# Kernel optimization log

Hardware: AMD Instinct MI355X
Metric: run time of the kernel (lower is better)

## Reference

```python
import jax, jax.numpy as jnp
import numpy as np

T, N, D_OBS = 32, 32, 64
HID, HEADS, MEM, N_ACT = 512, 4, 128, 16
SECTIONS = [HEADS * HID, HEADS, HID, 1, HID, HID, HEADS, 1, 1, 3 * HEADS]
XI = sum(SECTIONS)


def setup_inputs() -> dict:
    key = jax.random.key(0)
    ks = jax.random.split(key, 8)
    s = 0.02
    return {
        "inputs": jax.random.normal(ks[0], (T, N, D_OBS), jnp.float32),
        "w_ih": jax.random.normal(ks[1], (3 * HID, D_OBS), jnp.float32) * s,
        "w_hh": jax.random.normal(ks[2], (3 * HID, HID), jnp.float32) * s,
        "b_ih": jnp.zeros((3 * HID,), jnp.float32),
        "b_hh": jnp.zeros((3 * HID,), jnp.float32),
        "Wf": jax.random.normal(ks[3], (XI, HID), jnp.float32) * s,
        "bf": jnp.zeros((XI,), jnp.float32),
        "Wa": jax.random.normal(ks[4], (N_ACT, HID), jnp.float32) * s,
        "ba": jnp.zeros((N_ACT,), jnp.float32),
        "Wc": jax.random.normal(ks[5], (1, HID), jnp.float32) * s,
        "bc": jnp.zeros((1,), jnp.float32),
    }


def reference(inputs, w_ih, w_hh, b_ih, b_hh, Wf, bf, Wa, ba, Wc, bc):
    idx = np.cumsum(SECTIONS)[:-1]
    eps = 1e-8

    def step(carry, x_t):
        h, wr, u, ww, M, p, L = carry
        # --- GRU cell (torch convention) ---
        gi = x_t @ w_ih.T + b_ih
        gh = h @ w_hh.T + b_hh
        ir, iz, inn = jnp.split(gi, 3, axis=-1)
        hr, hz, hn = jnp.split(gh, 3, axis=-1)
        rg = jax.nn.sigmoid(ir + hr)
        zg = jax.nn.sigmoid(iz + hz)
        ng = jnp.tanh(inn + rg * hn)
        h = (1 - zg) * ng + zg * h
        # --- interface vector xi ---
        xi = jax.nn.relu(h) @ Wf.T + bf
        Kr, Br, kw, bw, e, v, F_hat, ga, gw, Pi = jnp.split(xi, idx, axis=-1)
        Kr = Kr.reshape(N, HEADS, HID)
        Br = jax.nn.softplus(Br)                      # [N,H]
        bw = jax.nn.softplus(bw)                      # [N,1]
        e = jax.nn.sigmoid(e)                         # [N,HID] erase
        v_w = v                                       # [N,HID] write vec
        F_hat = jax.nn.sigmoid(F_hat)                 # [N,H] free gates
        ga = jax.nn.sigmoid(ga)                       # [N,1]
        gw = jax.nn.sigmoid(gw)                       # [N,1]
        Pi = jax.nn.softmax(Pi.reshape(N, HEADS, 3), axis=-1)
        # --- memory retention & usage ---
        psi = jnp.prod(1 - F_hat[..., None] * wr, axis=1)          # [N,MEM]
        u = (u + ww - u * ww) * psi
        # --- allocation weighting via usage sort ---
        phi = jnp.argsort(u, axis=-1)
        u_sorted = jnp.take_along_axis(u, phi, axis=-1)
        excl = jnp.concatenate(
            [jnp.ones((N, 1), u.dtype), jnp.cumprod(u_sorted[:, :-1], axis=-1)], axis=-1)
        a_sorted = (1 - u_sorted) * excl
        alloc = jnp.zeros_like(u).at[jnp.arange(N)[:, None], phi].set(a_sorted)
        # --- content-based write weighting ---
        Mn = jnp.sqrt(jnp.sum(M * M, axis=-1))                     # [N,MEM]
        kwn = jnp.sqrt(jnp.sum(kw * kw, axis=-1, keepdims=True))   # [N,1]
        cos_w = jnp.einsum('nmd,nd->nm', M, kw) / (Mn * kwn + eps)
        cw = jax.nn.softmax(bw * cos_w, axis=-1)
        ww = gw * (ga * alloc + (1 - ga) * cw)                     # [N,MEM]
        # --- memory write (erase + add outer products) ---
        M = M * (1 - ww[..., None] * e[:, None, :]) + ww[..., None] * v_w[:, None, :]
        # --- precedence & temporal link matrix ---
        p = (1 - jnp.sum(ww, axis=-1, keepdims=True)) * p + ww
        L = (1 - ww[..., None] - ww[:, None, :]) * L + ww[..., None] * p[:, None, :]
        # --- forward/backward read weights ---
        fwd_w = jnp.einsum('nij,nhj->nhi', L, wr)
        bwd_w = jnp.einsum('nji,nhj->nhi', L, wr)
        # --- content-based read weighting ---
        Mn2 = jnp.sqrt(jnp.sum(M * M, axis=-1))                    # [N,MEM]
        Krn = jnp.sqrt(jnp.sum(Kr * Kr, axis=-1, keepdims=True))   # [N,H,1]
        cos_r = jnp.einsum('nmd,nhd->nhm', M, Kr) / (Mn2[:, None, :] * Krn + eps)
        cr = jax.nn.softmax(Br[..., None] * cos_r, axis=-1)
        wr = Pi[..., 0:1] * bwd_w + Pi[..., 1:2] * cr + Pi[..., 2:3] * fwd_w
        # --- read vectors, actor, critic ---
        r_read = jnp.einsum('nmd,nhm->nd', M, wr)                  # sum over heads -> [N,HID]
        a_probs = jax.nn.softmax(r_read @ Wa.T + ba, axis=-1)      # [N,N_ACT]
        val = h @ Wc.T + bc                                        # [N,1]
        return (h, wr, u, ww, M, p, L), jnp.concatenate([a_probs, val], axis=-1)

    z = jnp.zeros
    carry0 = (z((N, HID)), z((N, HEADS, MEM)), z((N, MEM)), z((N, MEM)),
              z((N, MEM, HID)), z((N, MEM)), z((N, MEM, MEM)))
    _, outs = jax.lax.scan(step, carry0, inputs)
    return outs  # [T, N, N_ACT+1]
```

## Files before the change

### kernel.cpp

```cpp
#include <hip/hip_runtime.h>
#include <math.h>

#define TT 32
#define NB 32
#define DOBS 64
#define HID 512
#define HEADS 4
#define MEM 128
#define NACT 16
#define XID 3607
#define G3 1536

__device__ __forceinline__ float sigm(float x){ return 1.0f/(1.0f+__expf(-x)); }
__device__ __forceinline__ float splus(float x){ return fmaxf(x,0.f) + log1pf(__expf(-fabsf(x))); }

__device__ __forceinline__ float wsum64(float s){
    s += __shfl_xor(s,1); s += __shfl_xor(s,2); s += __shfl_xor(s,4);
    s += __shfl_xor(s,8); s += __shfl_xor(s,16);
    float t = s;
    asm volatile("v_permlane32_swap_b32 %0, %1" : "+v"(s), "+v"(t));
    return s + t;
}
__device__ __forceinline__ float wmax64(float s){
    s = fmaxf(s, __shfl_xor(s,1)); s = fmaxf(s, __shfl_xor(s,2)); s = fmaxf(s, __shfl_xor(s,4));
    s = fmaxf(s, __shfl_xor(s,8)); s = fmaxf(s, __shfl_xor(s,16));
    float t = s;
    asm volatile("v_permlane32_swap_b32 %0, %1" : "+v"(s), "+v"(t));
    return fmaxf(s, t);
}

__global__ __launch_bounds__(256) void k_transpose(const float* __restrict__ src,
                                                   float* __restrict__ dst, int R, int C)
{
    __shared__ float tile[32][33];
    int r0 = blockIdx.x*32, c0 = blockIdx.y*32;
    int tx = threadIdx.x, ty = threadIdx.y;
    #pragma unroll
    for (int yy = 0; yy < 32; yy += 8) {
        int r = r0 + ty + yy, c = c0 + tx;
        if (r < R && c < C) tile[ty+yy][tx] = src[(size_t)r*C + c];
    }
    __syncthreads();
    #pragma unroll
    for (int yy = 0; yy < 32; yy += 8) {
        int c = c0 + ty + yy, r = r0 + tx;
        if (r < R && c < C) dst[(size_t)c*R + r] = tile[tx][ty+yy];
    }
}

__global__ __launch_bounds__(384) void k_gru(
    const float* __restrict__ x,
    const float* __restrict__ wihT,
    const float* __restrict__ whhT,
    const float* __restrict__ b_ih,
    const float* __restrict__ b_hh,
    float* __restrict__ h_all,
    float* hG,
    int* flags)
{
    const int n   = blockIdx.x & 31;
    const int s   = blockIdx.x >> 5;
    const int tid = threadIdx.x;
    const int kq  = tid / 96;
    const int c   = tid % 96;
    const int g   = c >> 5;
    const int r0  = g*512 + s*128 + (c & 31)*4;

    __shared__ float hS[512];
    __shared__ float xS[64];
    __shared__ float4 pI[4][96];
    __shared__ float4 pH[4][96];
    __shared__ float grS[128], gzS[128], giN[128], ghN[128];

    for (int i = tid; i < 512; i += 384) hS[i] = 0.f;

    for (int t = 0; t < TT; ++t) {
        if (tid < 64) xS[tid] = x[((size_t)t*NB + n)*DOBS + tid];
        __syncthreads();
        {
            float4 aI = make_float4(0.f,0.f,0.f,0.f);
            float4 aH = make_float4(0.f,0.f,0.f,0.f);
            const int kx0 = kq*16;
            #pragma unroll 4
            for (int k = kx0; k < kx0+16; ++k) {
                float xv = xS[k];
                float4 w = *(const float4*)(wihT + (size_t)k*G3 + r0);
                aI.x += w.x*xv; aI.y += w.y*xv; aI.z += w.z*xv; aI.w += w.w*xv;
            }
            const int kh0 = kq*128;
            #pragma unroll 4
            for (int k = kh0; k < kh0+128; ++k) {
                float hv = hS[k];
                float4 w = *(const float4*)(whhT + (size_t)k*G3 + r0);
                aH.x += w.x*hv; aH.y += w.y*hv; aH.z += w.z*hv; aH.w += w.w*hv;
            }
            pI[kq][c] = aI; pH[kq][c] = aH;
        }
        __syncthreads();
        {
            const int g2 = tid >> 7, d = tid & 127;
            const int c2 = g2*32 + (d>>2), e = d & 3;
            float AI = 0.f, AH = 0.f;
            #pragma unroll
            for (int q = 0; q < 4; ++q) {
                float4 vi = pI[q][c2], vh = pH[q][c2];
                AI += (e==0)?vi.x:(e==1)?vi.y:(e==2)?vi.z:vi.w;
                AH += (e==0)?vh.x:(e==1)?vh.y:(e==2)?vh.z:vh.w;
            }
            const int rg = g2*512 + s*128 + d;
            AI += b_ih[rg]; AH += b_hh[rg];
            if (g2 == 0)      grS[d] = AI + AH;
            else if (g2 == 1) gzS[d] = AI + AH;
            else              { giN[d] = AI; ghN[d] = AH; }
        }
        __syncthreads();
        if (tid < 128) {
            const int D = s*128 + tid;
            float rg = sigm(grS[tid]);
            float zg = sigm(gzS[tid]);
            float ng = tanhf(giN[tid] + rg*ghN[tid]);
            float hn = (1.f-zg)*ng + zg*hS[D];
            h_all[((size_t)t*NB + n)*HID + D] = hn;
            __hip_atomic_store(&hG[n*HID + D], hn, __ATOMIC_RELAXED, __HIP_MEMORY_SCOPE_AGENT);
        }
        __syncthreads();
        if (t+1 < TT) {
            if (tid == 0) {
                __hip_atomic_fetch_add(&flags[n], 1, __ATOMIC_RELEASE, __HIP_MEMORY_SCOPE_AGENT);
                while (__hip_atomic_load(&flags[n], __ATOMIC_ACQUIRE, __HIP_MEMORY_SCOPE_AGENT) < 4*(t+1)) {
                    __builtin_amdgcn_s_sleep(4);
                }
            }
            __syncthreads();
            for (int i = tid; i < 512; i += 384)
                hS[i] = __hip_atomic_load(&hG[n*HID + i], __ATOMIC_RELAXED, __HIP_MEMORY_SCOPE_AGENT);
        }
    }
}

__global__ __launch_bounds__(256) void k_xi(
    const float* __restrict__ h_all,
    const float* __restrict__ Wf,
    const float* __restrict__ bf,
    float* __restrict__ xi_all)
{
    __shared__ float As[16][132];
    __shared__ float Bs[16][68];
    const int jt = blockIdx.x * 64;
    const int it = blockIdx.y * 128;
    const int tid = threadIdx.x;
    const int lc = tid & 15, lr = tid >> 4;
    const int tx = tid & 15, ty = tid >> 4;
    float acc[8][4] = {};

    for (int k0 = 0; k0 < HID; k0 += 16) {
        #pragma unroll
        for (int s = 0; s < 8; ++s) {
            int i = lr*8 + s;
            As[lc][i] = fmaxf(h_all[(size_t)(it + i)*HID + k0 + lc], 0.f);
        }
        #pragma unroll
        for (int s = 0; s < 4; ++s) {
            int j = lr*4 + s;
            Bs[lc][j] = (jt + j < XID) ? Wf[(size_t)(jt + j)*HID + k0 + lc] : 0.f;
        }
        __syncthreads();
        #pragma unroll
        for (int k = 0; k < 16; ++k) {
            float a[8], b[4];
            #pragma unroll
            for (int u = 0; u < 8; ++u) a[u] = As[k][ty*8+u];
            #pragma unroll
            for (int v = 0; v < 4; ++v) b[v] = Bs[k][tx*4+v];
            #pragma unroll
            for (int u = 0; u < 8; ++u)
                #pragma unroll
                for (int v = 0; v < 4; ++v) acc[u][v] += a[u]*b[v];
        }
        __syncthreads();
    }
    #pragma unroll
    for (int u = 0; u < 8; ++u)
        #pragma unroll
        for (int v = 0; v < 4; ++v) {
            int i = it + ty*8 + u, j = jt + tx*4 + v;
            if (j < XID) xi_all[(size_t)i*XID + j] = acc[u][v] + bf[j];
        }
}

__global__ __launch_bounds__(64) void k_val(
    const float* __restrict__ h_all, const float* __restrict__ Wc,
    const float* __restrict__ bc, float* __restrict__ out)
{
    const int row = blockIdx.x;
    const int lane = threadIdx.x;
    float acc = 0.f;
    for (int d = lane; d < HID; d += 64) acc += h_all[(size_t)row*HID + d]*Wc[d];
    for (int off = 32; off; off >>= 1) acc += __shfl_down(acc, off);
    if (lane == 0) out[(size_t)row*17 + 16] = acc + bc[0];
}

#define LPAD 132
#define SROW 544
#define DYN_FLOATS (128*LPAD + 16*SROW)
#define CIDX(d) ((((d)>>6)*68) + ((d)&63))

__global__ __launch_bounds__(1024) void k_mem(
    const float* __restrict__ xi_all,
    const float* __restrict__ Wa,
    const float* __restrict__ ba,
    float* __restrict__ out)
{
    extern __shared__ __align__(16) float dynS[];
    float* Lm  = dynS;
    float* scr = dynS + 128*LPAD;

    const int n = blockIdx.x;
    const int tid = threadIdx.x;
    const int lane = tid & 63;
    const int wv = tid >> 6;
    const int m8 = tid >> 3;
    const int q8 = tid & 7;

    __shared__ __align__(16) float KrC[4*544];
    __shared__ __align__(16) float kwC[544], eC[544], vC[544];
    __shared__ __align__(16) float wrC[4*136];
    __shared__ __align__(16) float r_S[512];
    __shared__ float dotK_S[4][132], fwd_S[4][132], bwd_S[4][132];
    __shared__ float u_S[128], ww_S[128], p_S[128], cw_S[128], srt_S[128], aS_S[128];
    __shared__ float Mn2_S[128], dw_S[128];
    __shared__ int   rk_S[128];
    __shared__ float wred[16][6];
    __shared__ float scal_S[8];
    __shared__ float PiRaw[12];
    __shared__ float Pi_S[4][3], Br_S[4], KrN_S[4], F_S[4];
    __shared__ float ba_S[16], logit_S[16];

    float4 Mreg[16];
    #pragma unroll
    for (int i = 0; i < 16; ++i) Mreg[i] = make_float4(0.f,0.f,0.f,0.f);

    for (int i = tid; i < 128*LPAD; i += 1024) Lm[i] = 0.f;
    if (tid < 16) ba_S[tid] = ba[tid];
    if (tid < 128) { u_S[tid]=0.f; ww_S[tid]=0.f; p_S[tid]=0.f; Mn2_S[tid]=0.f; }
    if (tid < 512) wrC[(tid>>7)*136 + CIDX(tid&127)] = 0.f;

    float waR[8];
    #pragma unroll
    for (int j = 0; j < 8; ++j) waR[j] = Wa[(wv<<9) + lane + (j<<6)];

    const bool hasEx = (tid >= 1000 && tid < 1023);
    int exIdx = 0;
    if (tid >= 1000 && tid < 1004)      exIdx = 2048 + (tid - 1000);
    else if (tid == 1004)               exIdx = 2564;
    else if (tid >= 1005 && tid < 1023) exIdx = 3589 + (tid - 1005);

    const float* xi0 = xi_all + (size_t)n*XID;
    float pKrA = xi0[tid];
    float pKrB = xi0[1024 + tid];
    float pkw = 0.f, pv = 0.f, pe = 0.f;
    if (tid < 512) { pkw = xi0[2052 + tid]; pv = xi0[3077 + tid]; }
    else           { pe  = xi0[2565 + (tid - 512)]; }
    float pex = hasEx ? xi0[exIdx] : 0.f;
    __syncthreads();

    for (int t = 0; t < TT; ++t) {
        float scv = 0.f, ev2 = 0.f;

        {
            int d = tid & 511, hh = tid >> 9;
            int co = CIDX(d);
            KrC[hh*544 + co]     = pKrA;
            KrC[(2+hh)*544 + co] = pKrB;
        }
        if (tid < 512) { int co = CIDX(tid); kwC[co] = pkw; vC[co] = pv; }
        else { int s2 = tid - 512; int co = CIDX(s2); eC[co] = sigm(pe); }
        if (hasEx) {
            if (tid < 1004)      Br_S[tid-1000] = splus(pex);
            else if (tid==1004)  scal_S[0] = splus(pex);
            else if (tid < 1009) F_S[tid-1005] = sigm(pex);
            else if (tid==1009)  scal_S[1] = sigm(pex);
            else if (tid==1010)  scal_S[2] = sigm(pex);
            else                 PiRaw[tid-1011] = pex;
        }
        {
            float sA = wsum64(pKrA*pKrA);
            float sB = wsum64(pKrB*pKrB);
            float sK = wsum64(pkw*pkw);
            if (lane == 0) { wred[wv][0]=sA; wred[wv][1]=sB; wred[wv][2]=sK; }
        }
        {
            int tn = (t+1 < TT) ? (t+1) : t;
            const float* xin = xi_all + (size_t)(tn*NB + n)*XID;
            pKrA = xin[tid]; pKrB = xin[1024 + tid];
            if (tid < 512) { pkw = xin[2052 + tid]; pv = xin[3077 + tid]; }
            else           { pe  = xin[2565 + (tid - 512)]; }
            if (hasEx) pex = xin[exIdx];
        }
        __syncthreads();

        if (tid < 4) {
            float s = 0.f;
            #pragma unroll
            for (int w = 0; w < 8; ++w) s += wred[(tid&1)*8 + w][tid>>1];
            KrN_S[tid] = sqrtf(s);
        } else if (tid == 4) {
            float s = 0.f;
            #pragma unroll
            for (int w = 0; w < 8; ++w) s += wred[w][2];
            scal_S[3] = sqrtf(s);
        }
        if (tid < 128) {
            int co = CIDX(tid);
            float psi = (1.f - F_S[0]*wrC[co])      * (1.f - F_S[1]*wrC[136+co])
                      * (1.f - F_S[2]*wrC[272+co])  * (1.f - F_S[3]*wrC[408+co]);
            float uu = u_S[tid], w = ww_S[tid];
            u_S[tid] = (uu + w - uu*w)*psi;
        }
        {
            const float* kwp = kwC + q8*68;
            float dw = 0.f;
            #pragma unroll
            for (int c = 0; c < 16; ++c) {
                float4 x = Mreg[c];
                float4 kk = *(const float4*)(kwp + 4*c);
                dw += x.x*kk.x + x.y*kk.y + x.z*kk.z + x.w*kk.w;
            }
            dw += __shfl_xor(dw,1); dw += __shfl_xor(dw,2); dw += __shfl_xor(dw,4);
            if (q8 == 0) dw_S[m8] = dw;
        }
        __syncthreads();

        {
            float um = u_S[m8];
            int rk = 0;
            #pragma unroll
            for (int jj = 0; jj < 16; ++jj) {
                int j = jj*8 + q8;
                float uj = u_S[j];
                rk += (uj < um || (uj == um && j < m8)) ? 1 : 0;
            }
            rk += __shfl_xor(rk,1); rk += __shfl_xor(rk,2); rk += __shfl_xor(rk,4);
            if (q8 == 0) { rk_S[m8] = rk; srt_S[rk] = um; }
        }
        if (tid < 128) {
            float cwv = scal_S[0]*dw_S[tid]/(Mn2_S[tid]*scal_S[3] + 1e-8f);
            cw_S[tid] = cwv;
            float mx = wmax64(cwv);
            if (lane == 0) wred[wv][0] = mx;
        } else if (tid >= 136 && tid < 140) {
            int h = tid - 136;
            float p0 = PiRaw[3*h], p1 = PiRaw[3*h+1], p2 = PiRaw[3*h+2];
            float mx = fmaxf(p0, fmaxf(p1, p2));
            float e0=__expf(p0-mx), e1=__expf(p1-mx), e2=__expf(p2-mx);
            float s = e0+e1+e2;
            Pi_S[h][0]=e0/s; Pi_S[h][1]=e1/s; Pi_S[h][2]=e2/s;
        }
        __syncthreads();

        if (tid < 128) {
            float ev = __expf(cw_S[tid] - fmaxf(wred[0][0], wred[1][0]));
            cw_S[tid] = ev;
            float s = wsum64(ev);
            if (lane == 0) wred[wv][1] = s;
        }
        if (wv == 0) {
            float x0 = srt_S[2*lane], x1 = srt_S[2*lane+1];
            float pp = x0*x1;
            float sc = pp;
            #pragma unroll
            for (int off = 1; off < 64; off <<= 1) {
                float y = __shfl_up(sc, off);
                if (lane >= off) sc *= y;
            }
            float excl = __shfl_up(sc, 1);
            if (lane == 0) excl = 1.f;
            aS_S[2*lane]   = (1.f - x0)*excl;
            aS_S[2*lane+1] = (1.f - x1)*excl*x0;
        }
        __syncthreads();

        if (tid < 128) {
            float cwsum = wred[0][1] + wred[1][1];
            float alloc = aS_S[rk_S[tid]];
            float ga = scal_S[1], gw = scal_S[2];
            float w = gw*(ga*alloc + (1.f-ga)*cw_S[tid]/cwsum);
            ww_S[tid] = w;
            float s = wsum64(w);
            if (lane == 0) wred[wv][0] = s;
        }
        __syncthreads();

        if (tid < 128) {
            float sww = wred[0][0] + wred[1][0];
            p_S[tid] = (1.f - sww)*p_S[tid] + ww_S[tid];
        }
        {
            const int base = q8*68;
            const float* ep  = eC + base;
            const float* vp  = vC + base;
            const float* k0p = KrC + base;
            const float* k1p = KrC + 544 + base;
            const float* k2p = KrC + 1088 + base;
            const float* k3p = KrC + 1632 + base;
            float wwm = ww_S[m8];
            float nrm=0.f, d0=0.f, d1=0.f, d2=0.f, d3=0.f;
            #pragma unroll
            for (int c = 0; c < 16; ++c) {
                float4 x  = Mreg[c];
                float4 ee = *(const float4*)(ep + 4*c);
                float4 vv = *(const float4*)(vp + 4*c);
                x.x = x.x*(1.f - wwm*ee.x) + wwm*vv.x;
                x.y = x.y*(1.f - wwm*ee.y) + wwm*vv.y;
                x.z = x.z*(1.f - wwm*ee.z) + wwm*vv.z;
                x.w = x.w*(1.f - wwm*ee.w) + wwm*vv.w;
                Mreg[c] = x;
                nrm += x.x*x.x + x.y*x.y + x.z*x.z + x.w*x.w;
                float4 k0 = *(const float4*)(k0p + 4*c);
                float4 k1 = *(const float4*)(k1p + 4*c);
                float4 k2 = *(const float4*)(k2p + 4*c);
                float4 k3 = *(const float4*)(k3p + 4*c);
                d0 += x.x*k0.x + x.y*k0.y + x.z*k0.z + x.w*k0.w;
                d1 += x.x*k1.x + x.y*k1.y + x.z*k1.z + x.w*k1.w;
                d2 += x.x*k2.x + x.y*k2.y + x.z*k2.z + x.w*k2.w;
                d3 += x.x*k3.x + x.y*k3.y + x.z*k3.z + x.w*k3.w;
            }
            nrm += __shfl_xor(nrm,1); nrm += __shfl_xor(nrm,2); nrm += __shfl_xor(nrm,4);
            d0  += __shfl_xor(d0,1);  d0  += __shfl_xor(d0,2);  d0  += __shfl_xor(d0,4);
            d1  += __shfl_xor(d1,1);  d1  += __shfl_xor(d1,2);  d1  += __shfl_xor(d1,4);
            d2  += __shfl_xor(d2,1);  d2  += __shfl_xor(d2,2);  d2  += __shfl_xor(d2,4);
            d3  += __shfl_xor(d3,1);  d3  += __shfl_xor(d3,2);  d3  += __shfl_xor(d3,4);
            if (q8 == 4) Mn2_S[m8] = sqrtf(nrm);
            else if (q8 < 4) dotK_S[q8][m8] = (q8==0) ? d0 : ((q8==1) ? d1 : ((q8==2) ? d2 : d3));
        }
        __syncthreads();

        {
            const int j2 = tid & 127, w8 = tid >> 7;
            float wwj = ww_S[j2], pj = p_S[j2];
            float b0=0.f,b1=0.f,b2=0.f,b3=0.f;
            #pragma unroll
            for (int c2 = 0; c2 < 4; ++c2) {
                const int r0 = (w8<<4) + (c2<<2);
                const int bidx = CIDX(r0);
                float4 wwv = *(const float4*)&ww_S[r0];
                float4 w0v = *(const float4*)&wrC[bidx];
                float4 w1v = *(const float4*)&wrC[136+bidx];
                float4 w2v = *(const float4*)&wrC[272+bidx];
                float4 w3v = *(const float4*)&wrC[408+bidx];
                #pragma unroll
                for (int s4 = 0; s4 < 4; ++s4) {
                    int i2 = r0 + s4;
                    float wwi = (s4==0)?wwv.x:(s4==1)?wwv.y:(s4==2)?wwv.z:wwv.w;
                    float lold = Lm[i2*LPAD + j2];
                    float ln = (1.f - wwi - wwj)*lold + wwi*pj;
                    Lm[i2*LPAD + j2] = ln;
                    b0 += ln*((s4==0)?w0v.x:(s4==1)?w0v.y:(s4==2)?w0v.z:w0v.w);
                    b1 += ln*((s4==0)?w1v.x:(s4==1)?w1v.y:(s4==2)?w1v.z:w1v.w);
                    b2 += ln*((s4==0)?w2v.x:(s4==1)?w2v.y:(s4==2)?w2v.z:w2v.w);
                    b3 += ln*((s4==0)?w3v.x:(s4==1)?w3v.y:(s4==2)?w3v.z:w3v.w);
                }
            }
            float* sp = scr + w8*SROW + j2;
            sp[0]=b0; sp[132]=b1; sp[264]=b2; sp[396]=b3;
        }
        __syncthreads();

        if (tid < 512) {
            int h = tid>>7, mm = tid&127;
            float s = 0.f;
            #pragma unroll
            for (int g = 0; g < 8; ++g) s += scr[g*SROW + h*132 + mm];
            bwd_S[h][mm] = s;
        }
        {
            const float* Lr = Lm + m8*LPAD + q8*16;
            const int wb = ((q8>>2)*68) + ((q8&3)<<4);
            float f0=0.f,f1=0.f,f2=0.f,f3=0.f;
            #pragma unroll
            for (int c = 0; c < 4; ++c) {
                float4 lv = *(const float4*)(Lr + 4*c);
                float4 w0 = *(const float4*)&wrC[wb + 4*c];
                float4 w1 = *(const float4*)&wrC[136 + wb + 4*c];
                float4 w2 = *(const float4*)&wrC[272 + wb + 4*c];
                float4 w3 = *(const float4*)&wrC[408 + wb + 4*c];
                f0 += lv.x*w0.x + lv.y*w0.y + lv.z*w0.z + lv.w*w0.w;
                f1 += lv.x*w1.x + lv.y*w1.y + lv.z*w1.z + lv.w*w1.w;
                f2 += lv.x*w2.x + lv.y*w2.y + lv.z*w2.z + lv.w*w2.w;
                f3 += lv.x*w3.x + lv.y*w3.y + lv.z*w3.z + lv.w*w3.w;
            }
            f0 += __shfl_xor(f0,1); f0 += __shfl_xor(f0,2); f0 += __shfl_xor(f0,4);
            f1 += __shfl_xor(f1,1); f1 += __shfl_xor(f1,2); f1 += __shfl_xor(f1,4);
            f2 += __shfl_xor(f2,1); f2 += __shfl_xor(f2,2); f2 += __shfl_xor(f2,4);
            f3 += __shfl_xor(f3,1); f3 += __shfl_xor(f3,2); f3 += __shfl_xor(f3,4);
            if (q8 < 4) fwd_S[q8][m8] = (q8==0) ? f0 : ((q8==1) ? f1 : ((q8==2) ? f2 : f3));
        }
        if (tid < 512) {
            int h = tid>>7, mm = tid&127;
            scv = Br_S[h]*dotK_S[h][mm]/(Mn2_S[mm]*KrN_S[h] + 1e-8f);
            float mxv = wmax64(scv);
            if (lane == 0) wred[wv][0] = mxv;
        }
        __syncthreads();

        if (tid < 512) {
            int h = tid>>7;
            float hmax = fmaxf(wred[2*h][0], wred[2*h+1][0]);
            ev2 = __expf(scv - hmax);
            float s = wsum64(ev2);
            if (lane == 0) wred[wv][1] = s;
        }
        __syncthreads();

        if (tid < 512) {
            int h = tid>>7, mm = tid&127;
            float hsum = wred[2*h][1] + wred[2*h+1][1];
            float cr = ev2/hsum;
            wrC[h*136 + CIDX(mm)] = Pi_S[h][0]*bwd_S[h][mm] + Pi_S[h][1]*cr + Pi_S[h][2]*fwd_S[h][mm];
        }
        __syncthreads();

        {
            const int co = CIDX(m8);
            float srtm = wrC[co] + wrC[136+co] + wrC[272+co] + wrC[408+co];
            float* sp = scr + wv*SROW + q8*68 + ((lane>>5)<<1);
            #pragma unroll
            for (int c = 0; c < 16; ++c) {
                float v0 = srtm*Mreg[c].x;
                float v1 = srtm*Mreg[c].y;
                float v2 = srtm*Mreg[c].z;
                float v3 = srtm*Mreg[c].w;
                asm volatile("v_permlane32_swap_b32 %0, %1" : "+v"(v0), "+v"(v2));
                float A = v0 + v2;
                asm volatile("v_permlane32_swap_b32 %0, %1" : "+v"(v1), "+v"(v3));
                float B = v1 + v3;
                A += __shfl_xor(A, 8); A += __shfl_xor(A, 16);
                B += __shfl_xor(B, 8); B += __shfl_xor(B, 16);
                if ((lane & 31) < 8) *(float2*)(sp + 4*c) = make_float2(A, B);
            }
        }
        __syncthreads();

        if (tid < 512) {
            int off = ((tid>>6)*68) + (tid&63);
            float r = 0.f;
            #pragma unroll
            for (int w = 0; w < 16; ++w) r += scr[w*SROW + off];
            r_S[tid] = r;
        }
        __syncthreads();

        {
            float acc = 0.f;
            #pragma unroll
            for (int j = 0; j < 8; ++j) acc += waR[j]*r_S[lane + (j<<6)];
            acc = wsum64(acc);
            if (lane == 0) logit_S[wv] = acc + ba_S[wv];
        }
        __syncthreads();

        if (tid < 16) {
            float lg = logit_S[tid];
            float mx = lg;
            mx = fmaxf(mx, __shfl_xor(mx,1)); mx = fmaxf(mx, __shfl_xor(mx,2));
            mx = fmaxf(mx, __shfl_xor(mx,4)); mx = fmaxf(mx, __shfl_xor(mx,8));
            float ex2 = __expf(lg - mx);
            float s = ex2;
            s += __shfl_xor(s,1); s += __shfl_xor(s,2);
            s += __shfl_xor(s,4); s += __shfl_xor(s,8);
            out[(size_t)(t*NB + n)*17 + tid] = ex2/s;
        }
    }
}

extern "C" void kernel_launch(void* const* d_in, const int* in_sizes, int n_in,
                              void* d_out, int out_size, void* d_ws, size_t ws_size,
                              hipStream_t stream) {
    const float* inp  = (const float*)d_in[0];
    const float* w_ih = (const float*)d_in[1];
    const float* w_hh = (const float*)d_in[2];
    const float* b_ih = (const float*)d_in[3];
    const float* b_hh = (const float*)d_in[4];
    const float* Wf   = (const float*)d_in[5];
    const float* bf   = (const float*)d_in[6];
    const float* Wa   = (const float*)d_in[7];
    const float* ba   = (const float*)d_in[8];
    const float* Wc   = (const float*)d_in[9];
    const float* bc   = (const float*)d_in[10];
    float* out = (float*)d_out;

    float* ws = (float*)d_ws;
    float* wihT   = ws;
    float* whhT   = ws + 98304;
    float* h_all  = ws + 884736;
    float* xi_all = ws + 1409024;
    float* hG     = ws + 5102592;
    int*   flags  = (int*)(ws + 5119008);

    static int dynset = 0;
    if (!dynset) {
        hipFuncSetAttribute(reinterpret_cast<const void*>(k_mem),
                            hipFuncAttributeMaxDynamicSharedMemorySize,
                            DYN_FLOATS*4);
        dynset = 1;
    }

    hipMemsetAsync(flags, 0, NB*sizeof(int), stream);

    dim3 tb(32, 8);
    k_transpose<<<dim3(48, 2),  tb, 0, stream>>>(w_ih, wihT, G3, DOBS);
    k_transpose<<<dim3(48, 16), tb, 0, stream>>>(w_hh, whhT, G3, HID);
    k_gru<<<NB*4, 384, 0, stream>>>(inp, wihT, whhT, b_ih, b_hh, h_all, hG, flags);
    k_xi<<<dim3(57, 8), 256, 0, stream>>>(h_all, Wf, bf, xi_all);
    k_val<<<TT*NB, 64, 0, stream>>>(h_all, Wc, bc, out);
    k_mem<<<NB, 1024, DYN_FLOATS*4, stream>>>(xi_all, Wa, ba, out);
}
```

Before: 1.388 ms.

## Remap memory rows to two rows per thread and drop softmax max passes

Each thread now holds two memory rows over 32 columns instead of one row over 64 columns. The write/erase update, norms, key dot products and read-vector reductions are rewritten for this layout, using new padded shared buffers and a permlane16/32-based cross-half reduction. Separately, the write-content and read-content softmaxes no longer subtract the max, which removes a reduction phase and a block barrier per step. The cost is a risk of exp overflow if the scaled cosine scores become large.

New measurement: 1.273 ms. -8.3%, faster.

```diff
diff --git a/kernel.cpp b/kernel.cpp
--- a/kernel.cpp
+++ b/kernel.cpp
@@ -21,12 +21,13 @@
     asm volatile("v_permlane32_swap_b32 %0, %1" : "+v"(s), "+v"(t));
     return s + t;
 }
-__device__ __forceinline__ float wmax64(float s){
-    s = fmaxf(s, __shfl_xor(s,1)); s = fmaxf(s, __shfl_xor(s,2)); s = fmaxf(s, __shfl_xor(s,4));
-    s = fmaxf(s, __shfl_xor(s,8)); s = fmaxf(s, __shfl_xor(s,16));
-    float t = s;
-    asm volatile("v_permlane32_swap_b32 %0, %1" : "+v"(s), "+v"(t));
-    return fmaxf(s, t);
+__device__ __forceinline__ float rsum_hi(float v){
+    float t = v;
+    asm volatile("v_permlane16_swap_b32 %0, %1" : "+v"(v), "+v"(t));
+    v += t;
+    float t2 = v;
+    asm volatile("v_permlane32_swap_b32 %0, %1" : "+v"(v), "+v"(t2));
+    return v + t2;
 }
 
 __global__ __launch_bounds__(256) void k_transpose(const float* __restrict__ src,
@@ -201,9 +202,10 @@
 }
 
 #define LPAD 132
-#define SROW 544
-#define DYN_FLOATS (128*LPAD + 16*SROW)
+#define SROW2 576
+#define DYN_FLOATS (128*LPAD + 16*SROW2)
 #define CIDX(d) ((((d)>>6)*68) + ((d)&63))
+#define CIDX2(d) ((((d)>>5)*36) + ((d)&31))
 
 __global__ __launch_bounds__(1024) void k_mem(
     const float* __restrict__ xi_all,
@@ -221,9 +223,12 @@
     const int wv = tid >> 6;
     const int m8 = tid >> 3;
     const int q8 = tid & 7;
-
-    __shared__ __align__(16) float KrC[4*544];
-    __shared__ __align__(16) float kwC[544], eC[544], vC[544];
+    const int rp = tid >> 4;
+    const int ch = tid & 15;
+    const int r0 = rp*2, r1 = r0+1;
+
+    __shared__ __align__(16) float KrC[4*576];
+    __shared__ __align__(16) float kwC[576], eC[576], vC[576];
     __shared__ __align__(16) float wrC[4*136];
     __shared__ __align__(16) float r_S[512];
     __shared__ float dotK_S[4][132], fwd_S[4][132], bwd_S[4][132];
@@ -265,16 +270,16 @@
     __syncthreads();
 
     for (int t = 0; t < TT; ++t) {
-        float scv = 0.f, ev2 = 0.f;
+        float ev2 = 0.f;
 
         {
             int d = tid & 511, hh = tid >> 9;
-            int co = CIDX(d);
-            KrC[hh*544 + co]     = pKrA;
-            KrC[(2+hh)*544 + co] = pKrB;
-        }
-        if (tid < 512) { int co = CIDX(tid); kwC[co] = pkw; vC[co] = pv; }
-        else { int s2 = tid - 512; int co = CIDX(s2); eC[co] = sigm(pe); }
+            int co = CIDX2(d);
+            KrC[hh*576 + co]     = pKrA;
+            KrC[(2+hh)*576 + co] = pKrB;
+        }
+        if (tid < 512) { int co = CIDX2(tid); kwC[co] = pkw; vC[co] = pv; }
+        else { int s2 = tid - 512; eC[CIDX2(s2)] = sigm(pe); }
         if (hasEx) {
             if (tid < 1004)      Br_S[tid-1000] = splus(pex);
             else if (tid==1004)  scal_S[0] = splus(pex);
@@ -318,16 +323,18 @@
             u_S[tid] = (uu + w - uu*w)*psi;
         }
         {
-            const float* kwp = kwC + q8*68;
-            float dw = 0.f;
-            #pragma unroll
-            for (int c = 0; c < 16; ++c) {
-                float4 x = Mreg[c];
+            const float* kwp = kwC + ch*36;
+            float dw0 = 0.f, dw1 = 0.f;
+            #pragma unroll
+            for (int c = 0; c < 8; ++c) {
                 float4 kk = *(const float4*)(kwp + 4*c);
-                dw += x.x*kk.x + x.y*kk.y + x.z*kk.z + x.w*kk.w;
-            }
-            dw += __shfl_xor(dw,1); dw += __shfl_xor(dw,2); dw += __shfl_xor(dw,4);
-            if (q8 == 0) dw_S[m8] = dw;
+                float4 x0 = Mreg[c], x1 = Mreg[8+c];
+                dw0 += x0.x*kk.x + x0.y*kk.y + x0.z*kk.z + x0.w*kk.w;
+                dw1 += x1.x*kk.x + x1.y*kk.y + x1.z*kk.z + x1.w*kk.w;
+            }
+            dw0 += __shfl_xor(dw0,1); dw0 += __shfl_xor(dw0,2); dw0 += __shfl_xor(dw0,4); dw0 += __shfl_xor(dw0,8);
+            dw1 += __shfl_xor(dw1,1); dw1 += __shfl_xor(dw1,2); dw1 += __shfl_xor(dw1,4); dw1 += __shfl_xor(dw1,8);
+            if (ch == 0) { dw_S[r0] = dw0; dw_S[r1] = dw1; }
         }
         __syncthreads();
 
@@ -345,9 +352,10 @@
         }
         if (tid < 128) {
             float cwv = scal_S[0]*dw_S[tid]/(Mn2_S[tid]*scal_S[3] + 1e-8f);
-            cw_S[tid] = cwv;
-            float mx = wmax64(cwv);
-            if (lane == 0) wred[wv][0] = mx;
+            float ev = __expf(cwv);
+            cw_S[tid] = ev;
+            float s = wsum64(ev);
+            if (lane == 0) wred[wv][1] = s;
         } else if (tid >= 136 && tid < 140) {
             int h = tid - 136;
             float p0 = PiRaw[3*h], p1 = PiRaw[3*h+1], p2 = PiRaw[3*h+2];
@@ -358,12 +366,6 @@
         }
         __syncthreads();
 
-        if (tid < 128) {
-            float ev = __expf(cw_S[tid] - fmaxf(wred[0][0], wred[1][0]));
-            cw_S[tid] = ev;
-            float s = wsum64(ev);
-            if (lane == 0) wred[wv][1] = s;
-        }
         if (wv == 0) {
             float x0 = srt_S[2*lane], x1 = srt_S[2*lane+1];
             float pp = x0*x1;
@@ -396,42 +398,65 @@
             p_S[tid] = (1.f - sww)*p_S[tid] + ww_S[tid];
         }
         {
-            const int base = q8*68;
+            const int base = ch*36;
             const float* ep  = eC + base;
             const float* vp  = vC + base;
             const float* k0p = KrC + base;
-            const float* k1p = KrC + 544 + base;
-            const float* k2p = KrC + 1088 + base;
-            const float* k3p = KrC + 1632 + base;
-            float wwm = ww_S[m8];
-            float nrm=0.f, d0=0.f, d1=0.f, d2=0.f, d3=0.f;
-            #pragma unroll
-            for (int c = 0; c < 16; ++c) {
-                float4 x  = Mreg[c];
+            const float* k1p = KrC + 576 + base;
+            const float* k2p = KrC + 1152 + base;
+            const float* k3p = KrC + 1728 + base;
+            const float ww0 = ww_S[r0], ww1 = ww_S[r1];
+            float nrm0=0.f, nrm1=0.f;
+            float a0=0.f,a1=0.f,a2=0.f,a3=0.f;
+            float b0=0.f,b1=0.f,b2=0.f,b3=0.f;
+            #pragma unroll
+            for (int c = 0; c < 8; ++c) {
                 float4 ee = *(const float4*)(ep + 4*c);
                 float4 vv = *(const float4*)(vp + 4*c);
-                x.x = x.x*(1.f - wwm*ee.x) + wwm*vv.x;
-                x.y = x.y*(1.f - wwm*ee.y) + wwm*vv.y;
-                x.z = x.z*(1.f - wwm*ee.z) + wwm*vv.z;
-                x.w = x.w*(1.f - wwm*ee.w) + wwm*vv.w;
+                float4 x  = Mreg[c];
+                x.x = x.x*(1.f - ww0*ee.x) + ww0*vv.x;
+                x.y = x.y*(1.f - ww0*ee.y) + ww0*vv.y;
+                x.z = x.z*(1.f - ww0*ee.z) + ww0*vv.z;
+                x.w = x.w*(1.f - ww0*ee.w) + ww0*vv.w;
                 Mreg[c] = x;
-                nrm += x.x*x.x + x.y*x.y + x.z*x.z + x.w*x.w;
+                nrm0 += x.x*x.x + x.y*x.y + x.z*x.z + x.w*x.w;
+                float4 y  = Mreg[8+c];
+                y.x = y.x*(1.f - ww1*ee.x) + ww1*vv.x;
+                y.y = y.y*(1.f - ww1*ee.y) + ww1*vv.y;
+                y.z = y.z*(1.f - ww1*ee.z) + ww1*vv.z;
+                y.w = y.w*(1.f - ww1*ee.w) + ww1*vv.w;
+                Mreg[8+c] = y;
+                nrm1 += y.x*y.x + y.y*y.y + y.z*y.z + y.w*y.w;
                 float4 k0 = *(const float4*)(k0p + 4*c);
                 float4 k1 = *(const float4*)(k1p + 4*c);
                 float4 k2 = *(const float4*)(k2p + 4*c);
                 float4 k3 = *(const float4*)(k3p + 4*c);
-                d0 += x.x*k0.x + x.y*k0.y + x.z*k0.z + x.w*k0.w;
-                d1 += x.x*k1.x + x.y*k1.y + x.z*k1.z + x.w*k1.w;
-                d2 += x.x*k2.x + x.y*k2.y + x.z*k2.z + x.w*k2.w;
-                d3 += x.x*k3.x + x.y*k3.y + x.z*k3.z + x.w*k3.w;
-            }
-            nrm += __shfl_xor(nrm,1); nrm += __shfl_xor(nrm,2); nrm += __shfl_xor(nrm,4);
-            d0  += __shfl_xor(d0,1);  d0  += __shfl_xor(d0,2);  d0  += __shfl_xor(d0,4);
-            d1  += __shfl_xor(d1,1);  d1  += __shfl_xor(d1,2);  d1  += __shfl_xor(d1,4);
-            d2  += __shfl_xor(d2,1);  d2  += __shfl_xor(d2,2);  d2  += __shfl_xor(d2,4);
-            d3  += __shfl_xor(d3,1);  d3  += __shfl_xor(d3,2);  d3  += __shfl_xor(d3,4);
-            if (q8 == 4) Mn2_S[m8] = sqrtf(nrm);
-            else if (q8 < 4) dotK_S[q8][m8] = (q8==0) ? d0 : ((q8==1) ? d1 : ((q8==2) ? d2 : d3));
+                a0 += x.x*k0.x + x.y*k0.y + x.z*k0.z + x.w*k0.w;
+                a1 += x.x*k1.x + x.y*k1.y + x.z*k1.z + x.w*k1.w;
+                a2 += x.x*k2.x + x.y*k2.y + x.z*k2.z + x.w*k2.w;
+                a3 += x.x*k3.x + x.y*k3.y + x.z*k3.z + x.w*k3.w;
+                b0 += y.x*k0.x + y.y*k0.y + y.z*k0.z + y.w*k0.w;
+                b1 += y.x*k1.x + y.y*k1.y + y.z*k1.z + y.w*k1.w;
+                b2 += y.x*k2.x + y.y*k2.y + y.z*k2.z + y.w*k2.w;
+                b3 += y.x*k3.x + y.y*k3.y + y.z*k3.z + y.w*k3.w;
+            }
+            #pragma unroll
+            for (int mk = 1; mk < 16; mk <<= 1) {
+                nrm0 += __shfl_xor(nrm0,mk); nrm1 += __shfl_xor(nrm1,mk);
+                a0 += __shfl_xor(a0,mk); a1 += __shfl_xor(a1,mk);
+                a2 += __shfl_xor(a2,mk); a3 += __shfl_xor(a3,mk);
+                b0 += __shfl_xor(b0,mk); b1 += __shfl_xor(b1,mk);
+                b2 += __shfl_xor(b2,mk); b3 += __shfl_xor(b3,mk);
+            }
+            if (ch < 4) {
+                float dA = (ch==0)?a0:(ch==1)?a1:(ch==2)?a2:a3;
+                float dB = (ch==0)?b0:(ch==1)?b1:(ch==2)?b2:b3;
+                dotK_S[ch][r0] = dA;
+                dotK_S[ch][r1] = dB;
+            } else if (ch == 4) {
+                Mn2_S[r0] = sqrtf(nrm0);
+                Mn2_S[r1] = sqrtf(nrm1);
+            }
         }
         __syncthreads();
 
@@ -441,16 +466,16 @@
             float b0=0.f,b1=0.f,b2=0.f,b3=0.f;
             #pragma unroll
             for (int c2 = 0; c2 < 4; ++c2) {
-                const int r0 = (w8<<4) + (c2<<2);
-                const int bidx = CIDX(r0);
-                float4 wwv = *(const float4*)&ww_S[r0];
+                const int rr0 = (w8<<4) + (c2<<2);
+                const int bidx = CIDX(rr0);
+                float4 wwv = *(const float4*)&ww_S[rr0];
                 float4 w0v = *(const float4*)&wrC[bidx];
                 float4 w1v = *(const float4*)&wrC[136+bidx];
                 float4 w2v = *(const float4*)&wrC[272+bidx];
                 float4 w3v = *(const float4*)&wrC[408+bidx];
                 #pragma unroll
                 for (int s4 = 0; s4 < 4; ++s4) {
-                    int i2 = r0 + s4;
+                    int i2 = rr0 + s4;
                     float wwi = (s4==0)?wwv.x:(s4==1)?wwv.y:(s4==2)?wwv.z:wwv.w;
                     float lold = Lm[i2*LPAD + j2];
                     float ln = (1.f - wwi - wwj)*lold + wwi*pj;
@@ -461,7 +486,7 @@
                     b3 += ln*((s4==0)?w3v.x:(s4==1)?w3v.y:(s4==2)?w3v.z:w3v.w);
                 }
             }
-            float* sp = scr + w8*SROW + j2;
+            float* sp = scr + w8*SROW2 + j2;
             sp[0]=b0; sp[132]=b1; sp[264]=b2; sp[396]=b3;
         }
         __syncthreads();
@@ -470,7 +495,7 @@
             int h = tid>>7, mm = tid&127;
             float s = 0.f;
             #pragma unroll
-            for (int g = 0; g < 8; ++g) s += scr[g*SROW + h*132 + mm];
+            for (int g = 0; g < 8; ++g) s += scr[g*SROW2 + h*132 + mm];
             bwd_S[h][mm] = s;
         }
         {
@@ -497,16 +522,8 @@
         }
         if (tid < 512) {
             int h = tid>>7, mm = tid&127;
-            scv = Br_S[h]*dotK_S[h][mm]/(Mn2_S[mm]*KrN_S[h] + 1e-8f);
-            float mxv = wmax64(scv);
-            if (lane == 0) wred[wv][0] = mxv;
-        }
-        __syncthreads();
-
-        if (tid < 512) {
-            int h = tid>>7;
-            float hmax = fmaxf(wred[2*h][0], wred[2*h+1][0]);
-            ev2 = __expf(scv - hmax);
+            float scv = Br_S[h]*dotK_S[h][mm]/(Mn2_S[mm]*KrN_S[h] + 1e-8f);
+            ev2 = __expf(scv);
             float s = wsum64(ev2);
             if (lane == 0) wred[wv][1] = s;
         }
@@ -521,31 +538,27 @@
         __syncthreads();
 
         {
-            const int co = CIDX(m8);
-            float srtm = wrC[co] + wrC[136+co] + wrC[272+co] + wrC[408+co];
-            float* sp = scr + wv*SROW + q8*68 + ((lane>>5)<<1);
-            #pragma unroll
-            for (int c = 0; c < 16; ++c) {
-                float v0 = srtm*Mreg[c].x;
-                float v1 = srtm*Mreg[c].y;
-                float v2 = srtm*Mreg[c].z;
-                float v3 = srtm*Mreg[c].w;
-                asm volatile("v_permlane32_swap_b32 %0, %1" : "+v"(v0), "+v"(v2));
-                float A = v0 + v2;
-                asm volatile("v_permlane32_swap_b32 %0, %1" : "+v"(v1), "+v"(v3));
-                float B = v1 + v3;
-                A += __shfl_xor(A, 8); A += __shfl_xor(A, 16);
-                B += __shfl_xor(B, 8); B += __shfl_xor(B, 16);
-                if ((lane & 31) < 8) *(float2*)(sp + 4*c) = make_float2(A, B);
+            const int co0 = CIDX(r0), co1 = CIDX(r1);
+            float s0 = wrC[co0] + wrC[136+co0] + wrC[272+co0] + wrC[408+co0];
+            float s1 = wrC[co1] + wrC[136+co1] + wrC[272+co1] + wrC[408+co1];
+            float* sp = scr + wv*SROW2 + ch*36;
+            #pragma unroll
+            for (int c = 0; c < 8; ++c) {
+                float4 x = Mreg[c], y = Mreg[8+c];
+                float px = rsum_hi(s0*x.x + s1*y.x);
+                float py = rsum_hi(s0*x.y + s1*y.y);
+                float pz = rsum_hi(s0*x.z + s1*y.z);
+                float pw = rsum_hi(s0*x.w + s1*y.w);
+                if (lane < 16) *(float4*)(sp + 4*c) = make_float4(px,py,pz,pw);
             }
         }
         __syncthreads();
 
         if (tid < 512) {
-            int off = ((tid>>6)*68) + (tid&63);
+            int off = CIDX2(tid);
             float r = 0.f;
             #pragma unroll
-            for (int w = 0; w < 16; ++w) r += scr[w*SROW + off];
+            for (int w = 0; w < 16; ++w) r += scr[w*SROW2 + off];
             r_S[tid] = r;
         }
         __syncthreads();
```
